# Performance work log

Measured on AMD Instinct MI355X. Metric: run time of the kernel, lower is better.

## Reference

```python
import jax, jax.numpy as jnp
import numpy as np

VOXEL_SIZE = 0.4
H, W = 512, 1408
FOOT = jnp.array([-1.0, 0.0, 1.0], dtype=jnp.float32)  # 3x3 splat footprint
NUSC_FREQ = np.array([1163161, 2309034, 188743, 2997643, 20317180, 852476, 243808, 2457947, 497017, 2731022, 7224789, 214411435, 5565043, 63191967, 76098082, 128860031, 141625221, 2307405309], np.float64)


def setup_inputs() -> dict:
    key = jax.random.key(0)
    k1, k2, k3 = jax.random.split(key, 3)
    B, NC = 1, 6
    X, Y, Z, C = 200, 200, 16, 17
    voxel_feats = jax.random.normal(k1, (B, X, Y, Z, C), jnp.float32)
    density = jax.random.uniform(k2, (B, X, Y, Z, 1), jnp.float32)
    # regular voxel-center grid (get_presudo_xyz)
    pc_min = np.array([-40.0, -40.0, -1.0])
    xs = pc_min[0] + (np.arange(X) + 0.5) * VOXEL_SIZE
    ys = pc_min[1] + (np.arange(Y) + 0.5) * VOXEL_SIZE
    zs = pc_min[2] + (np.arange(Z) + 0.5) * VOXEL_SIZE
    Xg, Yg, Zg = np.meshgrid(xs, ys, zs, indexing='ij')
    pc_xyz = jnp.asarray(np.stack([Xg, Yg, Zg], -1).reshape(-1, 3), dtype=jnp.float32)
    # plausible world-to-camera extrinsics: identity rotation, scene pushed to depth ~50
    vm = np.tile(np.eye(4, dtype=np.float32), (B, NC, 1, 1))
    vm[..., 2, 3] = 50.0
    vm[:, :, 0, 3] = np.linspace(-2.0, 2.0, NC, dtype=np.float32)
    viewmats = jnp.asarray(vm)
    Kc = np.zeros((B, NC, 3, 3), np.float32)
    Kc[..., 0, 0] = 560.0; Kc[..., 1, 1] = 560.0
    Kc[..., 0, 2] = W / 2.0; Kc[..., 1, 2] = H / 2.0; Kc[..., 2, 2] = 1.0
    Ks = jnp.asarray(Kc)
    gt_sem = jax.random.randint(k3, (B, NC, H, W), 0, 17, dtype=jnp.int32)
    class_weights = jnp.asarray(1.0 / np.log(NUSC_FREQ[:17] + 0.001), jnp.float32)
    return dict(voxel_feats=voxel_feats, density=density, viewmats=viewmats, Ks=Ks,
                gt_sem=gt_sem, pc_xyz=pc_xyz, class_weights=class_weights)


def _render(viewmat, Kmat, xyz, feats, opac):
    """Differentiable gaussian splat onto an HxW feature image (additive compositing)."""
    R, t = viewmat[:3, :3], viewmat[:3, 3]
    p = xyz @ R.T + t                      # [N,3] camera space
    z = jnp.maximum(p[:, 2], 1e-3)
    fx, fy, cx, cy = Kmat[0, 0], Kmat[1, 1], Kmat[0, 2], Kmat[1, 2]
    u = fx * p[:, 0] / z + cx
    v = fy * p[:, 1] / z + cy
    s2 = VOXEL_SIZE * VOXEL_SIZE           # isotropic scale^2 (regular-grid KDTree dists)
    j00, j11 = fx / z, fy / z              # EWA projection Jacobian
    j02 = -fx * p[:, 0] / (z * z)
    j12 = -fy * p[:, 1] / (z * z)
    a = s2 * (j00 * j00 + j02 * j02) + 0.3  # 2D covariance + 0.3 pixel dilation (3DGS)
    b = s2 * (j02 * j12)
    c = s2 * (j11 * j11 + j12 * j12) + 0.3
    det = a * c - b * b
    ca, cb, cc = c / det, -b / det, a / det  # conic (inverse 2D covariance)
    px = jnp.round(u)[:, None, None] + FOOT[None, :, None]   # [N,3,3]
    py = jnp.round(v)[:, None, None] + FOOT[None, None, :]
    ddx = px - u[:, None, None]
    ddy = py - v[:, None, None]
    g = jnp.exp(-0.5 * (ca[:, None, None] * ddx * ddx
                        + 2.0 * cb[:, None, None] * ddx * ddy
                        + cc[:, None, None] * ddy * ddy))
    valid = ((p[:, 2] > 0.1)[:, None, None]
             & (px >= 0) & (px < W) & (py >= 0) & (py < H))
    wgt = jnp.where(valid, opac[:, None, None] * g, 0.0)     # [N,3,3]
    idx = (jnp.clip(py, 0, H - 1) * W + jnp.clip(px, 0, W - 1)).astype(jnp.int32).reshape(-1)
    contrib = (wgt[..., None] * feats[:, None, None, :]).reshape(-1, feats.shape[-1])
    return jax.ops.segment_sum(contrib, idx, num_segments=H * W)  # [H*W, C]


def reference(voxel_feats, density, viewmats, Ks, gt_sem, pc_xyz, class_weights):
    B, NC = voxel_feats.shape[0], viewmats.shape[1]
    C = voxel_feats.shape[-1]
    loss_b = jnp.float32(0.0)
    for b in range(B):
        feats = voxel_feats[b].reshape(-1, C)
        opac = density[b].reshape(-1)
        loss_c = jnp.float32(0.0)
        for cid in range(NC):
            logits = _render(viewmats[b, cid], Ks[b, cid], pc_xyz, feats, opac)
            gt = gt_sem[b, cid].reshape(-1)
            logp = jax.nn.log_softmax(logits, axis=-1)
            nll = -jnp.take_along_axis(logp, gt[:, None], axis=1)[:, 0]
            # masked, class-weighted CE, matching nn.CrossEntropyLoss(weight, 'mean')
            wvec = jnp.where(gt != 0, class_weights[gt], 0.0)
            loss_c = loss_c + jnp.sum(wvec * nll) / jnp.maximum(jnp.sum(wvec), 1e-8)
        loss_b = loss_b + loss_c / NC
    return loss_b / B  # gaussian_sem_weight = 1.0
```

## Files before the change

kernel.cpp:

```cpp
#include <hip/hip_runtime.h>
#include <hip/hip_fp16.h>

#define HH 512
#define WW 1408
#define HWPIX (HH*WW)
#define NCH 17
#define NX 200
#define NY 200
#define NZ 16
#define NVOX (NX*NY*NZ)
#define NCAM 6
#define VOXSZ 0.4f
#define PCMINX (-40.0f)
#define PCMINY (-40.0f)
#define PCMINZ (-1.0f)
#define S2 (VOXSZ*VOXSZ)

union U4H8 { uint4 u; __half2 h2[4]; __half h[8]; };

__global__ __launch_bounds__(256) void build_tables(
    const float* __restrict__ viewmats,
    const float* __restrict__ Ks,
    float2* __restrict__ xtab,
    float2* __restrict__ ytab,
    float4* __restrict__ ltab,
    float* __restrict__ accum)
{
    if (blockIdx.x == 0 && threadIdx.x < 16) accum[threadIdx.x] = 0.f;

    const int cam = blockIdx.x / NZ;
    const int iz  = blockIdx.x % NZ;
    const float* vm = viewmats + cam * 16;
    const float* K  = Ks + cam * 9;
    const float fx = K[0], fy = K[4], cx = K[2], cy = K[5];
    const float zw = PCMINZ + ((float)iz + 0.5f) * VOXSZ;
    const float pz = vm[10] * zw + vm[11];
    const bool layerok = pz > 0.1f;
    const float z = fmaxf(pz, 0.001f);
    const float invz = 1.0f / z;
    const float j00 = fx * invz, j11 = fy * invz;

    if (threadIdx.x == 0)
        ltab[cam * NZ + iz] = make_float4(S2 * invz * invz,
                                          S2 * j00 * j00,
                                          S2 * j11 * j11, 0.f);

    for (int px = threadIdx.x; px < WW; px += blockDim.x) {
        const float xt = ((float)px - cx) * z / fx - vm[3];
        const int ixe = (int)rintf((xt - PCMINX) * 2.5f - 0.5f);
        int sel = -1; float usel = 0.f;
        for (int d = -1; d <= 1; ++d) {
            const int ix = ixe + d;
            const float xw = PCMINX + ((float)ix + 0.5f) * VOXSZ;
            const float pxc = vm[0] * xw + vm[3];
            const float u = fx * pxc * invz + cx;
            if (ix >= 0 && ix < NX && fabsf((float)px - rintf(u)) <= 1.0f) {
                sel = ix; usel = u;
            }
        }
        if (!layerok) sel = -1;
        xtab[(cam * NZ + iz) * WW + px] = make_float2(usel, __int_as_float(sel));
    }
    for (int py = threadIdx.x; py < HH; py += blockDim.x) {
        const float yt = ((float)py - cy) * z / fy - vm[7];
        const int iye = (int)rintf((yt - PCMINY) * 2.5f - 0.5f);
        int sel = -1; float vsel = 0.f;
        for (int d = -1; d <= 1; ++d) {
            const int iy = iye + d;
            const float yw = PCMINY + ((float)iy + 0.5f) * VOXSZ;
            const float pyc = vm[5] * yw + vm[7];
            const float v = fy * pyc * invz + cy;
            if (iy >= 0 && iy < NY && fabsf((float)py - rintf(v)) <= 1.0f) {
                sel = iy; vsel = v;
            }
        }
        if (!layerok) sel = -1;
        ytab[(cam * NZ + iz) * HH + py] = make_float2(vsel, __int_as_float(sel));
    }
}

#define TIX 20
__global__ __launch_bounds__(256) void transpose_kernel(
    const float* __restrict__ feats,
    const float* __restrict__ density,
    uint4*  __restrict__ h4tab,
    __half* __restrict__ h1tab)
{
    __shared__ float ldsF[TIX][273];
    __shared__ float ldsD[TIX][NZ];
    const int t = threadIdx.x;
    const int iy     = blockIdx.x / 10;
    const int ixBase = (blockIdx.x % 10) * TIX;

    for (int q = t; q < TIX * 272; q += 256) {
        const int r = q / 272, j = q % 272;
        ldsF[r][j] = feats[((size_t)(ixBase + r) * NY + iy) * 272 + j];
    }
    for (int q = t; q < TIX * NZ; q += 256) {
        const int r = q / NZ, iz = q % NZ;
        ldsD[r][iz] = density[((size_t)(ixBase + r) * NY + iy) * NZ + iz];
    }
    __syncthreads();

    for (int q = t; q < 2 * NZ * TIX; q += 256) {
        const int r  = q % TIX;
        const int pz = q / TIX;
        const int iz = pz >> 1;
        const int kg = pz & 1;
        const float d = ldsD[r][iz];
        const int j = iz * NCH + kg * 8;
        U4H8 pk;
        #pragma unroll
        for (int i = 0; i < 8; ++i) pk.h[i] = __float2half(ldsF[r][j + i] * d);
        h4tab[(size_t)kg * NVOX + (iz * NY + iy) * NX + ixBase + r] = pk.u;
    }
    for (int q = t; q < NZ * TIX; q += 256) {
        const int r  = q % TIX;
        const int iz = q / TIX;
        h1tab[(iz * NY + iy) * NX + ixBase + r] =
            __float2half(ldsF[r][iz * NCH + 16] * ldsD[r][iz]);
    }
}

__global__ __launch_bounds__(256) void gather_loss_kernel(
    const uint4*  __restrict__ h4tab,
    const __half* __restrict__ h1tab,
    const float2* __restrict__ xtab,
    const float2* __restrict__ ytab,
    const float4* __restrict__ ltab,
    const int*    __restrict__ gt,
    const float*  __restrict__ cw,
    const float*  __restrict__ Ks,
    float* __restrict__ accum)
{
    const int pix = blockIdx.x * blockDim.x + threadIdx.x;
    const int cam0 = blockIdx.y * 2;
    const int px = pix % WW;
    const int py = pix / WW;
    const float pxF = (float)px, pyF = (float)py;

    const float cx = Ks[2], cy = Ks[5];

    const float2* xb0 = xtab + (size_t)((cam0 + 0) * NZ) * WW + px;
    const float2* xb1 = xtab + (size_t)((cam0 + 1) * NZ) * WW + px;
    const float2* yb0 = ytab + (size_t)((cam0 + 0) * NZ) * HH + py;
    const float2* yb1 = ytab + (size_t)((cam0 + 1) * NZ) * HH + py;
    const float4* lb0 = ltab + (cam0 + 0) * NZ;
    const float4* lb1 = ltab + (cam0 + 1) * NZ;

    float acc[2][NCH];
    #pragma unroll
    for (int c2 = 0; c2 < 2; ++c2)
        #pragma unroll
        for (int k = 0; k < NCH; ++k) acc[c2][k] = 0.f;

    float2 xe0 = xb0[0], xe1 = xb1[0];
    float2 ye0 = yb0[0], ye1 = yb1[0];
    float4 le0 = lb0[0], le1 = lb1[0];

    #pragma unroll 1
    for (int iz = 0; iz < NZ; ++iz) {
        const float2 xc0 = xe0, xc1 = xe1, yc0 = ye0, yc1 = ye1;
        const float4 lc0 = le0, lc1 = le1;
        const int izn = (iz + 1 < NZ) ? iz + 1 : iz;
        xe0 = xb0[(size_t)izn * WW];  xe1 = xb1[(size_t)izn * WW];
        ye0 = yb0[(size_t)izn * HH];  ye1 = yb1[(size_t)izn * HH];
        le0 = lb0[izn];               le1 = lb1[izn];

        #pragma unroll
        for (int c2 = 0; c2 < 2; ++c2) {
            const float2 xe = c2 ? xc1 : xc0;
            const float2 ye = c2 ? yc1 : yc0;
            const float4 lt = c2 ? lc1 : lc0;
            const int ix = __float_as_int(xe.y);
            const int iy = __float_as_int(ye.y);
            if ((ix | iy) >= 0) {
                const float gx = cx - xe.x;
                const float gy = cy - ye.x;
                const float a = lt.y + lt.x * gx * gx + 0.3f;
                const float b = lt.x * gx * gy;
                const float c = lt.z + lt.x * gy * gy + 0.3f;
                const float invdet = 1.0f / (a * c - b * b);
                const float du = pxF - xe.x;
                const float dv = pyF - ye.x;
                const float q = c * du * du - 2.f * b * du * dv + a * dv * dv;
                const float w = __expf(-0.5f * q * invdet);
                const int viT = (iz * NY + iy) * NX + ix;
                U4H8 p0, p1;
                p0.u = h4tab[viT];
                p1.u = h4tab[(size_t)NVOX + viT];
                const float fs = __half2float(h1tab[viT]);
                #pragma unroll
                for (int i = 0; i < 4; ++i) {
                    const float2 lo = __half22float2(p0.h2[i]);
                    acc[c2][2*i + 0] = fmaf(w, lo.x, acc[c2][2*i + 0]);
                    acc[c2][2*i + 1] = fmaf(w, lo.y, acc[c2][2*i + 1]);
                    const float2 hi = __half22float2(p1.h2[i]);
                    acc[c2][8 + 2*i + 0] = fmaf(w, hi.x, acc[c2][8 + 2*i + 0]);
                    acc[c2][8 + 2*i + 1] = fmaf(w, hi.y, acc[c2][8 + 2*i + 1]);
                }
                acc[c2][16] = fmaf(w, fs, acc[c2][16]);
            }
        }
    }

    float wnll[2], wsum[2];
    #pragma unroll
    for (int c2 = 0; c2 < 2; ++c2) {
        const int cam = cam0 + c2;
        float m = acc[c2][0];
        #pragma unroll
        for (int k = 1; k < NCH; ++k) m = fmaxf(m, acc[c2][k]);
        float s = 0.f;
        #pragma unroll
        for (int k = 0; k < NCH; ++k) s += __expf(acc[c2][k] - m);
        const float lse = m + __logf(s);

        const int g = gt[(size_t)cam * HWPIX + pix];
        float selLogit = 0.f;
        #pragma unroll
        for (int k = 0; k < NCH; ++k)
            selLogit = (g == k) ? acc[c2][k] : selLogit;

        const float wvt = (g != 0) ? cw[g] : 0.f;
        wnll[c2] = wvt * (lse - selLogit);
        wsum[c2] = wvt;
    }

    #pragma unroll
    for (int off = 32; off > 0; off >>= 1) {
        #pragma unroll
        for (int c2 = 0; c2 < 2; ++c2) {
            wnll[c2] += __shfl_down(wnll[c2], off);
            wsum[c2] += __shfl_down(wsum[c2], off);
        }
    }
    __shared__ float red[4][4];
    const int wave = threadIdx.x >> 6, lane = threadIdx.x & 63;
    if (lane == 0) {
        #pragma unroll
        for (int c2 = 0; c2 < 2; ++c2) {
            red[wave][c2 * 2 + 0] = wnll[c2];
            red[wave][c2 * 2 + 1] = wsum[c2];
        }
    }
    __syncthreads();
    if (threadIdx.x < 4) {
        const float v = red[0][threadIdx.x] + red[1][threadIdx.x] +
                        red[2][threadIdx.x] + red[3][threadIdx.x];
        atomicAdd(&accum[cam0 * 2 + threadIdx.x], v);
    }
}

__global__ void finalize_kernel(const float* __restrict__ accum, float* __restrict__ out)
{
    if (threadIdx.x == 0 && blockIdx.x == 0) {
        float loss = 0.f;
        for (int c = 0; c < NCAM; ++c)
            loss += accum[c * 2 + 0] / fmaxf(accum[c * 2 + 1], 1e-8f);
        out[0] = loss / (float)NCAM;
    }
}

extern "C" void kernel_launch(void* const* d_in, const int* in_sizes, int n_in,
                              void* d_out, int out_size, void* d_ws, size_t ws_size,
                              hipStream_t stream)
{
    const float* voxel_feats = (const float*)d_in[0];
    const float* density     = (const float*)d_in[1];
    const float* viewmats    = (const float*)d_in[2];
    const float* Ks          = (const float*)d_in[3];
    const int*   gt_sem      = (const int*)  d_in[4];
    const float* pc_xyz      = (const float*)d_in[5];  (void)pc_xyz;
    const float* cw          = (const float*)d_in[6];
    float* out = (float*)d_out;

    char* w = (char*)d_ws;
    float*  accum = (float*)w;                          w += 256;
    float2* xtab  = (float2*)w;                         w += (size_t)NCAM * NZ * WW * sizeof(float2);
    float2* ytab  = (float2*)w;                         w += (size_t)NCAM * NZ * HH * sizeof(float2);
    float4* ltab  = (float4*)w;                         w += ((size_t)NCAM * NZ * sizeof(float4) + 255) & ~255ULL;
    uint4*  h4tab = (uint4*)w;                          w += (size_t)2 * NVOX * sizeof(uint4);
    __half* h1tab = (__half*)w;

    build_tables<<<NCAM * NZ, 256, 0, stream>>>(viewmats, Ks, xtab, ytab, ltab, accum);
    transpose_kernel<<<NY * 10, 256, 0, stream>>>(voxel_feats, density, h4tab, h1tab);

    dim3 grid(HWPIX / 256, 3);
    gather_loss_kernel<<<grid, 256, 0, stream>>>(h4tab, h1tab, xtab, ytab, ltab,
                                                 gt_sem, cw, Ks, accum);
    finalize_kernel<<<1, 64, 0, stream>>>(accum, out);
}
```

Baseline: 247.0 us.

## Merge prep kernels, fold finalize into gather, process three cameras per thread

Combines the table-building and voxel transpose kernels into one launch with block-range dispatch, and folds the finalize step into the gather kernel using a last-block-done counter. The gather kernel now handles three cameras per thread instead of two, splitting the z loop into a weight-computation phase and a feature-gather phase so more independent loads can be in flight. The intent is to cut launch overhead and improve memory-level parallelism. In exchange it raises register pressure from 51 accumulators, which may lower occupancy, and it drops the explicit next-layer prefetch of the x/y table entries.

```diff
diff --git a/kernel.cpp b/kernel.cpp
--- a/kernel.cpp
+++ b/kernel.cpp
@@ -15,21 +15,67 @@
 #define PCMINY (-40.0f)
 #define PCMINZ (-1.0f)
 #define S2 (VOXSZ*VOXSZ)
+#define TIX 20
+#define NPREP_T (NY*10)
+#define NGATHER_BLOCKS ((HWPIX/256)*2)
 
 union U4H8 { uint4 u; __half2 h2[4]; __half h[8]; };
 
-__global__ __launch_bounds__(256) void build_tables(
+__global__ __launch_bounds__(256) void prep_kernel(
+    const float* __restrict__ feats,
+    const float* __restrict__ density,
     const float* __restrict__ viewmats,
     const float* __restrict__ Ks,
+    uint4*  __restrict__ h4tab,
+    __half* __restrict__ h1tab,
     float2* __restrict__ xtab,
     float2* __restrict__ ytab,
     float4* __restrict__ ltab,
-    float* __restrict__ accum)
+    float* __restrict__ accum,
+    unsigned int* __restrict__ counter)
 {
-    if (blockIdx.x == 0 && threadIdx.x < 16) accum[threadIdx.x] = 0.f;
-
-    const int cam = blockIdx.x / NZ;
-    const int iz  = blockIdx.x % NZ;
+    const int t = threadIdx.x;
+    if (blockIdx.x < NPREP_T) {
+        __shared__ float ldsF[TIX][273];
+        __shared__ float ldsD[TIX][NZ];
+        const int iy     = blockIdx.x / 10;
+        const int ixBase = (blockIdx.x % 10) * TIX;
+        for (int q = t; q < TIX * 272; q += 256) {
+            const int r = q / 272, j = q % 272;
+            ldsF[r][j] = feats[((size_t)(ixBase + r) * NY + iy) * 272 + j];
+        }
+        for (int q = t; q < TIX * NZ; q += 256) {
+            const int r = q / NZ, iz = q % NZ;
+            ldsD[r][iz] = density[((size_t)(ixBase + r) * NY + iy) * NZ + iz];
+        }
+        __syncthreads();
+        for (int q = t; q < 2 * NZ * TIX; q += 256) {
+            const int r  = q % TIX;
+            const int pz = q / TIX;
+            const int iz = pz >> 1;
+            const int kg = pz & 1;
+            const float d = ldsD[r][iz];
+            const int j = iz * NCH + kg * 8;
+            U4H8 pk;
+            #pragma unroll
+            for (int i = 0; i < 8; ++i) pk.h[i] = __float2half(ldsF[r][j + i] * d);
+            h4tab[(size_t)kg * NVOX + (iz * NY + iy) * NX + ixBase + r] = pk.u;
+        }
+        for (int q = t; q < NZ * TIX; q += 256) {
+            const int r  = q % TIX;
+            const int iz = q / TIX;
+            h1tab[(iz * NY + iy) * NX + ixBase + r] =
+                __float2half(ldsF[r][iz * NCH + 16] * ldsD[r][iz]);
+        }
+        return;
+    }
+
+    const int bid = blockIdx.x - NPREP_T;
+    if (bid == 0 && t < 16) accum[t] = 0.f;
+    if (bid == 0 && t == 0) *counter = 0u;
+
+    const int cam = bid / NZ;
+    const int iz  = bid % NZ;
     const float* vm = viewmats + cam * 16;
     const float* K  = Ks + cam * 9;
     const float fx = K[0], fy = K[4], cx = K[2], cy = K[5];
@@ -40,12 +86,12 @@
     const float invz = 1.0f / z;
     const float j00 = fx * invz, j11 = fy * invz;
 
-    if (threadIdx.x == 0)
+    if (t == 0)
         ltab[cam * NZ + iz] = make_float4(S2 * invz * invz,
                                           S2 * j00 * j00,
                                           S2 * j11 * j11, 0.f);
 
-    for (int px = threadIdx.x; px < WW; px += blockDim.x) {
+    for (int px = t; px < WW; px += blockDim.x) {
         const float xt = ((float)px - cx) * z / fx - vm[3];
         const int ixe = (int)rintf((xt - PCMINX) * 2.5f - 0.5f);
         int sel = -1; float usel = 0.f;
@@ -61,7 +107,7 @@
         if (!layerok) sel = -1;
         xtab[(cam * NZ + iz) * WW + px] = make_float2(usel, __int_as_float(sel));
     }
-    for (int py = threadIdx.x; py < HH; py += blockDim.x) {
+    for (int py = t; py < HH; py += blockDim.x) {
         const float yt = ((float)py - cy) * z / fy - vm[7];
         const int iye = (int)rintf((yt - PCMINY) * 2.5f - 0.5f);
         int sel = -1; float vsel = 0.f;
@@ -79,49 +125,6 @@
     }
 }
 
-#define TIX 20
-__global__ __launch_bounds__(256) void transpose_kernel(
-    const float* __restrict__ feats,
-    const float* __restrict__ density,
-    uint4*  __restrict__ h4tab,
-    __half* __restrict__ h1tab)
-{
-    __shared__ float ldsF[TIX][273];
-    __shared__ float ldsD[TIX][NZ];
-    const int t = threadIdx.x;
-    const int iy     = blockIdx.x / 10;
-    const int ixBase = (blockIdx.x % 10) * TIX;
-
-    for (int q = t; q < TIX * 272; q += 256) {
-        const int r = q / 272, j = q % 272;
-        ldsF[r][j] = feats[((size_t)(ixBase + r) * NY + iy) * 272 + j];
-    }
-    for (int q = t; q < TIX * NZ; q += 256) {
-        const int r = q / NZ, iz = q % NZ;
-        ldsD[r][iz] = density[((size_t)(ixBase + r) * NY + iy) * NZ + iz];
-    }
-    __syncthreads();
-
-    for (int q = t; q < 2 * NZ * TIX; q += 256) {
-        const int r  = q % TIX;
-        const int pz = q / TIX;
-        const int iz = pz >> 1;
-        const int kg = pz & 1;
-        const float d = ldsD[r][iz];
-        const int j = iz * NCH + kg * 8;
-        U4H8 pk;
-        #pragma unroll
-        for (int i = 0; i < 8; ++i) pk.h[i] = __float2half(ldsF[r][j + i] * d);
-        h4tab[(size_t)kg * NVOX + (iz * NY + iy) * NX + ixBase + r] = pk.u;
-    }
-    for (int q = t; q < NZ * TIX; q += 256) {
-        const int r  = q % TIX;
-        const int iz = q / TIX;
-        h1tab[(iz * NY + iy) * NX + ixBase + r] =
-            __float2half(ldsF[r][iz * NCH + 16] * ldsD[r][iz]);
-    }
-}
-
 __global__ __launch_bounds__(256) void gather_loss_kernel(
     const uint4*  __restrict__ h4tab,
     const __half* __restrict__ h1tab,
@@ -131,61 +134,54 @@
     const int*    __restrict__ gt,
     const float*  __restrict__ cw,
     const float*  __restrict__ Ks,
-    float* __restrict__ accum)
+    float* __restrict__ accum,
+    unsigned int* __restrict__ counter,
+    float* __restrict__ out)
 {
     const int pix = blockIdx.x * blockDim.x + threadIdx.x;
-    const int cam0 = blockIdx.y * 2;
+    const int cam0 = blockIdx.y * 3;
     const int px = pix % WW;
     const int py = pix / WW;
     const float pxF = (float)px, pyF = (float)py;
 
     const float cx = Ks[2], cy = Ks[5];
 
-    const float2* xb0 = xtab + (size_t)((cam0 + 0) * NZ) * WW + px;
-    const float2* xb1 = xtab + (size_t)((cam0 + 1) * NZ) * WW + px;
-    const float2* yb0 = ytab + (size_t)((cam0 + 0) * NZ) * HH + py;
-    const float2* yb1 = ytab + (size_t)((cam0 + 1) * NZ) * HH + py;
-    const float4* lb0 = ltab + (cam0 + 0) * NZ;
-    const float4* lb1 = ltab + (cam0 + 1) * NZ;
-
-    float acc[2][NCH];
+    float acc[3][NCH];
     #pragma unroll
-    for (int c2 = 0; c2 < 2; ++c2)
-        #pragma unroll
-        for (int k = 0; k < NCH; ++k) acc[c2][k] = 0.f;
-
-    float2 xe0 = xb0[0], xe1 = xb1[0];
-    float2 ye0 = yb0[0], ye1 = yb1[0];
-    float4 le0 = lb0[0], le1 = lb1[0];
+    for (int c = 0; c < 3; ++c)
+        #pragma unroll
+        for (int k = 0; k < NCH; ++k) acc[c][k] = 0.f;
 
     #pragma unroll 1
     for (int iz = 0; iz < NZ; ++iz) {
-        const float2 xc0 = xe0, xc1 = xe1, yc0 = ye0, yc1 = ye1;
-        const float4 lc0 = le0, lc1 = le1;
-        const int izn = (iz + 1 < NZ) ? iz + 1 : iz;
-        xe0 = xb0[(size_t)izn * WW];  xe1 = xb1[(size_t)izn * WW];
-        ye0 = yb0[(size_t)izn * HH];  ye1 = yb1[(size_t)izn * HH];
-        le0 = lb0[izn];               le1 = lb1[izn];
-
-        #pragma unroll
-        for (int c2 = 0; c2 < 2; ++c2) {
-            const float2 xe = c2 ? xc1 : xc0;
-            const float2 ye = c2 ? yc1 : yc0;
-            const float4 lt = c2 ? lc1 : lc0;
+        float wv[3]; int vi[3];
+        #pragma unroll
+        for (int c = 0; c < 3; ++c) {
+            const int cam = cam0 + c;
+            const float2 xe = xtab[(size_t)(cam * NZ + iz) * WW + px];
+            const float2 ye = ytab[(size_t)(cam * NZ + iz) * HH + py];
+            const float4 lt = ltab[cam * NZ + iz];
             const int ix = __float_as_int(xe.y);
             const int iy = __float_as_int(ye.y);
-            if ((ix | iy) >= 0) {
-                const float gx = cx - xe.x;
-                const float gy = cy - ye.x;
-                const float a = lt.y + lt.x * gx * gx + 0.3f;
-                const float b = lt.x * gx * gy;
-                const float c = lt.z + lt.x * gy * gy + 0.3f;
-                const float invdet = 1.0f / (a * c - b * b);
-                const float du = pxF - xe.x;
-                const float dv = pyF - ye.x;
-                const float q = c * du * du - 2.f * b * du * dv + a * dv * dv;
-                const float w = __expf(-0.5f * q * invdet);
-                const int viT = (iz * NY + iy) * NX + ix;
+            const bool cov = (ix | iy) >= 0;
+            const float gx = cx - xe.x;
+            const float gy = cy - ye.x;
+            const float a = lt.y + lt.x * gx * gx + 0.3f;
+            const float b = lt.x * gx * gy;
+            const float cc = lt.z + lt.x * gy * gy + 0.3f;
+            const float invdet = 1.0f / (a * cc - b * b);
+            const float du = pxF - xe.x;
+            const float dv = pyF - ye.x;
+            const float q = cc * du * du - 2.f * b * du * dv + a * dv * dv;
+            const float w = __expf(-0.5f * q * invdet);
+            wv[c] = cov ? w : 0.f;
+            vi[c] = cov ? (iz * NY + iy) * NX + ix : -1;
+        }
+        #pragma unroll
+        for (int c = 0; c < 3; ++c) {
+            if (vi[c] >= 0) {
+                const int viT = vi[c];
+                const float w = wv[c];
                 U4H8 p0, p1;
                 p0.u = h4tab[viT];
                 p1.u = h4tab[(size_t)NVOX + viT];
@@ -193,72 +189,77 @@
                 #pragma unroll
                 for (int i = 0; i < 4; ++i) {
                     const float2 lo = __half22float2(p0.h2[i]);
-                    acc[c2][2*i + 0] = fmaf(w, lo.x, acc[c2][2*i + 0]);
-                    acc[c2][2*i + 1] = fmaf(w, lo.y, acc[c2][2*i + 1]);
+                    acc[c][2*i + 0] = fmaf(w, lo.x, acc[c][2*i + 0]);
+                    acc[c][2*i + 1] = fmaf(w, lo.y, acc[c][2*i + 1]);
                     const float2 hi = __half22float2(p1.h2[i]);
-                    acc[c2][8 + 2*i + 0] = fmaf(w, hi.x, acc[c2][8 + 2*i + 0]);
-                    acc[c2][8 + 2*i + 1] = fmaf(w, hi.y, acc[c2][8 + 2*i + 1]);
+                    acc[c][8 + 2*i + 0] = fmaf(w, hi.x, acc[c][8 + 2*i + 0]);
+                    acc[c][8 + 2*i + 1] = fmaf(w, hi.y, acc[c][8 + 2*i + 1]);
                 }
-                acc[c2][16] = fmaf(w, fs, acc[c2][16]);
-            }
-        }
-    }
-
-    float wnll[2], wsum[2];
+                acc[c][16] = fmaf(w, fs, acc[c][16]);
+            }
+        }
+    }
+
+    float wnll[3], wsum[3];
     #pragma unroll
-    for (int c2 = 0; c2 < 2; ++c2) {
-        const int cam = cam0 + c2;
-        float m = acc[c2][0];
-        #pragma unroll
-        for (int k = 1; k < NCH; ++k) m = fmaxf(m, acc[c2][k]);
+    for (int c = 0; c < 3; ++c) {
+        const int cam = cam0 + c;
+        float m = acc[c][0];
+        #pragma unroll
+        for (int k = 1; k < NCH; ++k) m = fmaxf(m, acc[c][k]);
         float s = 0.f;
         #pragma unroll
-        for (int k = 0; k < NCH; ++k) s += __expf(acc[c2][k] - m);
+        for (int k = 0; k < NCH; ++k) s += __expf(acc[c][k] - m);
         const float lse = m + __logf(s);
 
         const int g = gt[(size_t)cam * HWPIX + pix];
         float selLogit = 0.f;
         #pragma unroll
         for (int k = 0; k < NCH; ++k)
-            selLogit = (g == k) ? acc[c2][k] : selLogit;
+            selLogit = (g == k) ? acc[c][k] : selLogit;
 
         const float wvt = (g != 0) ? cw[g] : 0.f;
-        wnll[c2] = wvt * (lse - selLogit);
-        wsum[c2] = wvt;
+        wnll[c] = wvt * (lse - selLogit);
+        wsum[c] = wvt;
     }
 
     #pragma unroll
     for (int off = 32; off > 0; off >>= 1) {
         #pragma unroll
-        for (int c2 = 0; c2 < 2; ++c2) {
-            wnll[c2] += __shfl_down(wnll[c2], off);
-            wsum[c2] += __shfl_down(wsum[c2], off);
-        }
-    }
-    __shared__ float red[4][4];
+        for (int c = 0; c < 3; ++c) {
+            wnll[c] += __shfl_down(wnll[c], off);
+            wsum[c] += __shfl_down(wsum[c], off);
+        }
+    }
+    __shared__ float red[4][6];
     const int wave = threadIdx.x >> 6, lane = threadIdx.x & 63;
     if (lane == 0) {
         #pragma unroll
-        for (int c2 = 0; c2 < 2; ++c2) {
-            red[wave][c2 * 2 + 0] = wnll[c2];
-            red[wave][c2 * 2 + 1] = wsum[c2];
+        for (int c = 0; c < 3; ++c) {
+            red[wave][c * 2 + 0] = wnll[c];
+            red[wave][c * 2 + 1] = wsum[c];
         }
     }
     __syncthreads();
-    if (threadIdx.x < 4) {
+    if (threadIdx.x < 6) {
         const float v = red[0][threadIdx.x] + red[1][threadIdx.x] +
                         red[2][threadIdx.x] + red[3][threadIdx.x];
         atomicAdd(&accum[cam0 * 2 + threadIdx.x], v);
     }
-}
-
-__global__ void finalize_kernel(const float* __restrict__ accum, float* __restrict__ out)
-{
-    if (threadIdx.x == 0 && blockIdx.x == 0) {
-        float loss = 0.f;
-        for (int c = 0; c < NCAM; ++c)
-            loss += accum[c * 2 + 0] / fmaxf(accum[c * 2 + 1], 1e-8f);
-        out[0] = loss / (float)NCAM;
+    __syncthreads();
+    if (threadIdx.x == 0) {
+        __threadfence();
+        const unsigned int done = atomicAdd(counter, 1u);
+        if (done == NGATHER_BLOCKS - 1) {
+            __threadfence();
+            float loss = 0.f;
+            for (int c2 = 0; c2 < NCAM; ++c2) {
+                const float n = atomicAdd(&accum[c2 * 2 + 0], 0.f);
+                const float d = atomicAdd(&accum[c2 * 2 + 1], 0.f);
+                loss += n / fmaxf(d, 1e-8f);
+            }
+            out[0] = loss / (float)NCAM;
+        }
     }
 }
 
@@ -276,18 +277,19 @@
     float* out = (float*)d_out;
 
     char* w = (char*)d_ws;
-    float*  accum = (float*)w;                          w += 256;
+    float*        accum   = (float*)w;
+    unsigned int* counter = (unsigned int*)(w + 64);    w += 256;
     float2* xtab  = (float2*)w;                         w += (size_t)NCAM * NZ * WW * sizeof(float2);
     float2* ytab  = (float2*)w;                         w += (size_t)NCAM * NZ * HH * sizeof(float2);
     float4* ltab  = (float4*)w;                         w += ((size_t)NCAM * NZ * sizeof(float4) + 255) & ~255ULL;
     uint4*  h4tab = (uint4*)w;                          w += (size_t)2 * NVOX * sizeof(uint4);
     __half* h1tab = (__half*)w;
 
-    build_tables<<<NCAM * NZ, 256, 0, stream>>>(viewmats, Ks, xtab, ytab, ltab, accum);
-    transpose_kernel<<<NY * 10, 256, 0, stream>>>(voxel_feats, density, h4tab, h1tab);
-
-    dim3 grid(HWPIX / 256, 3);
+    prep_kernel<<<NPREP_T + NCAM * NZ, 256, 0, stream>>>(
+        voxel_feats, density, viewmats, Ks, h4tab, h1tab,
+        xtab, ytab, ltab, accum, counter);
+
+    dim3 grid(HWPIX / 256, 2);
     gather_loss_kernel<<<grid, 256, 0, stream>>>(h4tab, h1tab, xtab, ytab, ltab,
-                                                 gt_sem, cw, Ks, accum);
-    finalize_kernel<<<1, 64, 0, stream>>>(accum, out);
+                                                 gt_sem, cw, Ks, accum, counter, out);
 }
```

Result: slower. 361.3 us (+46.3%).

## Fuse prep kernels, precompute covariance terms, interleave feature halves, finalize in last block

Applied to the files above, without the earlier changes.

Merges the table-building and feature-transpose kernels into one launch, and folds the finalize step into the gather kernel through a last-block atomic counter. This cuts the launch count from four to two. The x/y tables grow to float4 and now carry precomputed conic terms (a, c and a sqrt factor for b), so the gather loop drops the per-layer ltab load and several multiplies. The two 8-half feature chunks of each voxel are interleaved so one gather reads adjacent 16-byte words. In exchange, the x/y tables double in size and the kernel relies on a threadfence/atomic-counter pattern for correctness.

```diff
diff --git a/kernel.cpp b/kernel.cpp
--- a/kernel.cpp
+++ b/kernel.cpp
@@ -15,21 +15,63 @@
 #define PCMINY (-40.0f)
 #define PCMINZ (-1.0f)
 #define S2 (VOXSZ*VOXSZ)
+#define TIX 20
+#define NPREP_T (NY*10)
+#define NGATHER_BLOCKS ((HWPIX/256)*3)
 
 union U4H8 { uint4 u; __half2 h2[4]; __half h[8]; };
 
-__global__ __launch_bounds__(256) void build_tables(
+__global__ __launch_bounds__(256) void prep_kernel(
+    const float* __restrict__ feats,
+    const float* __restrict__ density,
     const float* __restrict__ viewmats,
     const float* __restrict__ Ks,
-    float2* __restrict__ xtab,
-    float2* __restrict__ ytab,
-    float4* __restrict__ ltab,
-    float* __restrict__ accum)
+    uint4*  __restrict__ h4tab,
+    __half* __restrict__ h1tab,
+    float4* __restrict__ xtab,
+    float4* __restrict__ ytab,
+    float* __restrict__ accum,
+    unsigned int* __restrict__ counter)
 {
-    if (blockIdx.x == 0 && threadIdx.x < 16) accum[threadIdx.x] = 0.f;
-
-    const int cam = blockIdx.x / NZ;
-    const int iz  = blockIdx.x % NZ;
+    const int t = threadIdx.x;
+    if (blockIdx.x < NPREP_T) {
+        __shared__ float ldsF[TIX][273];
+        __shared__ float ldsD[TIX][NZ];
+        const int iy     = blockIdx.x / 10;
+        const int ixBase = (blockIdx.x % 10) * TIX;
+        for (int q = t; q < TIX * 272; q += 256) {
+            const int r = q / 272, j = q % 272;
+            ldsF[r][j] = feats[((size_t)(ixBase + r) * NY + iy) * 272 + j];
+        }
+        for (int q = t; q < TIX * NZ; q += 256) {
+            const int r = q / NZ, iz = q % NZ;
+            ldsD[r][iz] = density[((size_t)(ixBase + r) * NY + iy) * NZ + iz];
+        }
+        __syncthreads();
+        for (int q = t; q < NZ * TIX; q += 256) {
+            const int r  = q % TIX;
+            const int iz = q / TIX;
+            const float d = ldsD[r][iz];
+            const int jb = iz * NCH;
+            const int viT = (iz * NY + iy) * NX + ixBase + r;
+            U4H8 p0, p1;
+            #pragma unroll
+            for (int i = 0; i < 8; ++i) p0.h[i] = __float2half(ldsF[r][jb + i] * d);
+            #pragma unroll
+            for (int i = 0; i < 8; ++i) p1.h[i] = __float2half(ldsF[r][jb + 8 + i] * d);
+            h4tab[(size_t)viT * 2 + 0] = p0.u;
+            h4tab[(size_t)viT * 2 + 1] = p1.u;
+            h1tab[viT] = __float2half(ldsF[r][jb + 16] * d);
+        }
+        return;
+    }
+
+    const int bid = blockIdx.x - NPREP_T;
+    if (bid == 0 && t < 16) accum[t] = 0.f;
+    if (bid == 0 && t == 0) *counter = 0u;
+
+    const int cam = bid / NZ;
+    const int iz  = bid % NZ;
     const float* vm = viewmats + cam * 16;
     const float* K  = Ks + cam * 9;
     const float fx = K[0], fy = K[4], cx = K[2], cy = K[5];
@@ -39,13 +81,12 @@
     const float z = fmaxf(pz, 0.001f);
     const float invz = 1.0f / z;
     const float j00 = fx * invz, j11 = fy * invz;
-
-    if (threadIdx.x == 0)
-        ltab[cam * NZ + iz] = make_float4(S2 * invz * invz,
-                                          S2 * j00 * j00,
-                                          S2 * j11 * j11, 0.f);
-
-    for (int px = threadIdx.x; px < WW; px += blockDim.x) {
+    const float lx  = S2 * invz * invz;
+    const float sq  = sqrtf(lx);
+    const float ay  = S2 * j00 * j00;
+    const float cyy = S2 * j11 * j11;
+
+    for (int px = t; px < WW; px += blockDim.x) {
         const float xt = ((float)px - cx) * z / fx - vm[3];
         const int ixe = (int)rintf((xt - PCMINX) * 2.5f - 0.5f);
         int sel = -1; float usel = 0.f;
@@ -59,9 +100,11 @@
             }
         }
         if (!layerok) sel = -1;
-        xtab[(cam * NZ + iz) * WW + px] = make_float2(usel, __int_as_float(sel));
-    }
-    for (int py = threadIdx.x; py < HH; py += blockDim.x) {
+        const float gx = cx - usel;
+        xtab[(cam * NZ + iz) * WW + px] =
+            make_float4(usel, ay + lx * gx * gx + 0.3f, sq * gx, __int_as_float(sel));
+    }
+    for (int py = t; py < HH; py += blockDim.x) {
         const float yt = ((float)py - cy) * z / fy - vm[7];
         const int iye = (int)rintf((yt - PCMINY) * 2.5f - 0.5f);
         int sel = -1; float vsel = 0.f;
@@ -75,63 +118,22 @@
             }
         }
         if (!layerok) sel = -1;
-        ytab[(cam * NZ + iz) * HH + py] = make_float2(vsel, __int_as_float(sel));
-    }
-}
-
-#define TIX 20
-__global__ __launch_bounds__(256) void transpose_kernel(
-    const float* __restrict__ feats,
-    const float* __restrict__ density,
-    uint4*  __restrict__ h4tab,
-    __half* __restrict__ h1tab)
-{
-    __shared__ float ldsF[TIX][273];
-    __shared__ float ldsD[TIX][NZ];
-    const int t = threadIdx.x;
-    const int iy     = blockIdx.x / 10;
-    const int ixBase = (blockIdx.x % 10) * TIX;
-
-    for (int q = t; q < TIX * 272; q += 256) {
-        const int r = q / 272, j = q % 272;
-        ldsF[r][j] = feats[((size_t)(ixBase + r) * NY + iy) * 272 + j];
-    }
-    for (int q = t; q < TIX * NZ; q += 256) {
-        const int r = q / NZ, iz = q % NZ;
-        ldsD[r][iz] = density[((size_t)(ixBase + r) * NY + iy) * NZ + iz];
-    }
-    __syncthreads();
-
-    for (int q = t; q < 2 * NZ * TIX; q += 256) {
-        const int r  = q % TIX;
-        const int pz = q / TIX;
-        const int iz = pz >> 1;
-        const int kg = pz & 1;
-        const float d = ldsD[r][iz];
-        const int j = iz * NCH + kg * 8;
-        U4H8 pk;
-        #pragma unroll
-        for (int i = 0; i < 8; ++i) pk.h[i] = __float2half(ldsF[r][j + i] * d);
-        h4tab[(size_t)kg * NVOX + (iz * NY + iy) * NX + ixBase + r] = pk.u;
-    }
-    for (int q = t; q < NZ * TIX; q += 256) {
-        const int r  = q % TIX;
-        const int iz = q / TIX;
-        h1tab[(iz * NY + iy) * NX + ixBase + r] =
-            __float2half(ldsF[r][iz * NCH + 16] * ldsD[r][iz]);
+        const float gy = cy - vsel;
+        ytab[(cam * NZ + iz) * HH + py] =
+            make_float4(vsel, cyy + lx * gy * gy + 0.3f, sq * gy, __int_as_float(sel));
     }
 }
 
 __global__ __launch_bounds__(256) void gather_loss_kernel(
     const uint4*  __restrict__ h4tab,
     const __half* __restrict__ h1tab,
-    const float2* __restrict__ xtab,
-    const float2* __restrict__ ytab,
-    const float4* __restrict__ ltab,
+    const float4* __restrict__ xtab,
+    const float4* __restrict__ ytab,
     const int*    __restrict__ gt,
     const float*  __restrict__ cw,
-    const float*  __restrict__ Ks,
-    float* __restrict__ accum)
+    float* __restrict__ accum,
+    unsigned int* __restrict__ counter,
+    float* __restrict__ out)
 {
     const int pix = blockIdx.x * blockDim.x + threadIdx.x;
     const int cam0 = blockIdx.y * 2;
@@ -139,14 +141,10 @@
     const int py = pix / WW;
     const float pxF = (float)px, pyF = (float)py;
 
-    const float cx = Ks[2], cy = Ks[5];
-
-    const float2* xb0 = xtab + (size_t)((cam0 + 0) * NZ) * WW + px;
-    const float2* xb1 = xtab + (size_t)((cam0 + 1) * NZ) * WW + px;
-    const float2* yb0 = ytab + (size_t)((cam0 + 0) * NZ) * HH + py;
-    const float2* yb1 = ytab + (size_t)((cam0 + 1) * NZ) * HH + py;
-    const float4* lb0 = ltab + (cam0 + 0) * NZ;
-    const float4* lb1 = ltab + (cam0 + 1) * NZ;
+    const float4* xb0 = xtab + (size_t)((cam0 + 0) * NZ) * WW + px;
+    const float4* xb1 = xtab + (size_t)((cam0 + 1) * NZ) * WW + px;
+    const float4* yb0 = ytab + (size_t)((cam0 + 0) * NZ) * HH + py;
+    const float4* yb1 = ytab + (size_t)((cam0 + 1) * NZ) * HH + py;
 
     float acc[2][NCH];
     #pragma unroll
@@ -154,41 +152,33 @@
         #pragma unroll
         for (int k = 0; k < NCH; ++k) acc[c2][k] = 0.f;
 
-    float2 xe0 = xb0[0], xe1 = xb1[0];
-    float2 ye0 = yb0[0], ye1 = yb1[0];
-    float4 le0 = lb0[0], le1 = lb1[0];
+    float4 xe0 = xb0[0], xe1 = xb1[0];
+    float4 ye0 = yb0[0], ye1 = yb1[0];
 
     #pragma unroll 1
     for (int iz = 0; iz < NZ; ++iz) {
-        const float2 xc0 = xe0, xc1 = xe1, yc0 = ye0, yc1 = ye1;
-        const float4 lc0 = le0, lc1 = le1;
+        const float4 xc0 = xe0, xc1 = xe1, yc0 = ye0, yc1 = ye1;
         const int izn = (iz + 1 < NZ) ? iz + 1 : iz;
         xe0 = xb0[(size_t)izn * WW];  xe1 = xb1[(size_t)izn * WW];
         ye0 = yb0[(size_t)izn * HH];  ye1 = yb1[(size_t)izn * HH];
-        le0 = lb0[izn];               le1 = lb1[izn];
 
         #pragma unroll
         for (int c2 = 0; c2 < 2; ++c2) {
-            const float2 xe = c2 ? xc1 : xc0;
-            const float2 ye = c2 ? yc1 : yc0;
-            const float4 lt = c2 ? lc1 : lc0;
-            const int ix = __float_as_int(xe.y);
-            const int iy = __float_as_int(ye.y);
+            const float4 xe = c2 ? xc1 : xc0;
+            const float4 ye = c2 ? yc1 : yc0;
+            const int ix = __float_as_int(xe.w);
+            const int iy = __float_as_int(ye.w);
             if ((ix | iy) >= 0) {
-                const float gx = cx - xe.x;
-                const float gy = cy - ye.x;
-                const float a = lt.y + lt.x * gx * gx + 0.3f;
-                const float b = lt.x * gx * gy;
-                const float c = lt.z + lt.x * gy * gy + 0.3f;
-                const float invdet = 1.0f / (a * c - b * b);
+                const float b = xe.z * ye.z;
+                const float invdet = 1.0f / (xe.y * ye.y - b * b);
                 const float du = pxF - xe.x;
                 const float dv = pyF - ye.x;
-                const float q = c * du * du - 2.f * b * du * dv + a * dv * dv;
+                const float q = xe.y * dv * dv - 2.f * b * du * dv + ye.y * du * du;
                 const float w = __expf(-0.5f * q * invdet);
                 const int viT = (iz * NY + iy) * NX + ix;
                 U4H8 p0, p1;
-                p0.u = h4tab[viT];
-                p1.u = h4tab[(size_t)NVOX + viT];
+                p0.u = h4tab[(size_t)viT * 2 + 0];
+                p1.u = h4tab[(size_t)viT * 2 + 1];
                 const float fs = __half2float(h1tab[viT]);
                 #pragma unroll
                 for (int i = 0; i < 4; ++i) {
@@ -250,15 +240,20 @@
                         red[2][threadIdx.x] + red[3][threadIdx.x];
         atomicAdd(&accum[cam0 * 2 + threadIdx.x], v);
     }
-}
-
-__global__ void finalize_kernel(const float* __restrict__ accum, float* __restrict__ out)
-{
-    if (threadIdx.x == 0 && blockIdx.x == 0) {
-        float loss = 0.f;
-        for (int c = 0; c < NCAM; ++c)
-            loss += accum[c * 2 + 0] / fmaxf(accum[c * 2 + 1], 1e-8f);
-        out[0] = loss / (float)NCAM;
+    __syncthreads();
+    if (threadIdx.x == 0) {
+        __threadfence();
+        const unsigned int done = atomicAdd(counter, 1u);
+        if (done == NGATHER_BLOCKS - 1) {
+            __threadfence();
+            float loss = 0.f;
+            for (int c = 0; c < NCAM; ++c) {
+                const float n = atomicAdd(&accum[c * 2 + 0], 0.f);
+                const float d = atomicAdd(&accum[c * 2 + 1], 0.f);
+                loss += n / fmaxf(d, 1e-8f);
+            }
+            out[0] = loss / (float)NCAM;
+        }
     }
 }
 
@@ -276,18 +271,18 @@
     float* out = (float*)d_out;
 
     char* w = (char*)d_ws;
-    float*  accum = (float*)w;                          w += 256;
-    float2* xtab  = (float2*)w;                         w += (size_t)NCAM * NZ * WW * sizeof(float2);
-    float2* ytab  = (float2*)w;                         w += (size_t)NCAM * NZ * HH * sizeof(float2);
-    float4* ltab  = (float4*)w;                         w += ((size_t)NCAM * NZ * sizeof(float4) + 255) & ~255ULL;
+    float*        accum   = (float*)w;
+    unsigned int* counter = (unsigned int*)(w + 64);    w += 256;
+    float4* xtab  = (float4*)w;                         w += (size_t)NCAM * NZ * WW * sizeof(float4);
+    float4* ytab  = (float4*)w;                         w += (size_t)NCAM * NZ * HH * sizeof(float4);
     uint4*  h4tab = (uint4*)w;                          w += (size_t)2 * NVOX * sizeof(uint4);
     __half* h1tab = (__half*)w;
 
-    build_tables<<<NCAM * NZ, 256, 0, stream>>>(viewmats, Ks, xtab, ytab, ltab, accum);
-    transpose_kernel<<<NY * 10, 256, 0, stream>>>(voxel_feats, density, h4tab, h1tab);
+    prep_kernel<<<NPREP_T + NCAM * NZ, 256, 0, stream>>>(
+        voxel_feats, density, viewmats, Ks, h4tab, h1tab,
+        xtab, ytab, accum, counter);
 
     dim3 grid(HWPIX / 256, 3);
-    gather_loss_kernel<<<grid, 256, 0, stream>>>(h4tab, h1tab, xtab, ytab, ltab,
-                                                 gt_sem, cw, Ks, accum);
-    finalize_kernel<<<1, 64, 0, stream>>>(accum, out);
+    gather_loss_kernel<<<grid, 256, 0, stream>>>(h4tab, h1tab, xtab, ytab,
+                                                 gt_sem, cw, accum, counter, out);
 }
```

New measurement: 445.8 us. 80.5% more time.
